# Optimization experiments

Measured on AMD Instinct MI355X. Metric: run time of the kernel, lower is better.

## Reference

```python
import jax, jax.numpy as jnp
import numpy as np

B, S, D, H, E = 4, 1024, 1024, 16, 4
HD = D // H
FF = 4 * D
EPS = 1e-5


def _ln(x):
    # normalize only; per-expert affine applied by caller
    mu = jnp.mean(x, axis=-1, keepdims=True)
    var = jnp.mean(jnp.square(x - mu), axis=-1, keepdims=True)
    return (x - mu) * jax.lax.rsqrt(var + EPS)


def setup_inputs() -> dict:
    key = jax.random.key(0)
    ks = jax.random.split(key, 12)
    s = 0.02
    inp = {
        "x": jax.random.normal(ks[0], (B, S, D), jnp.float32),
        # attention router
        "Wr_a": jax.random.normal(ks[1], (D, E), jnp.float32) * s,
        "br_a": jnp.zeros((E,), jnp.float32),
        # per-expert attention params
        "g_a": jnp.ones((E, D), jnp.float32),
        "b_a": jnp.zeros((E, D), jnp.float32),
        "Wqkv": jax.random.normal(ks[2], (E, D, 3 * D), jnp.float32) * s,
        "bqkv": jnp.zeros((E, 3 * D), jnp.float32),
        "Wpr": jax.random.normal(ks[3], (E, D, D), jnp.float32) * s,
        "bpr": jnp.zeros((E, D), jnp.float32),
        # MLP router
        "Wr_m": jax.random.normal(ks[4], (D, E), jnp.float32) * s,
        "br_m": jnp.zeros((E,), jnp.float32),
        # per-expert MLP params
        "g_m": jnp.ones((E, D), jnp.float32),
        "b_m": jnp.zeros((E, D), jnp.float32),
        "Wfc": jax.random.normal(ks[5], (E, D, FF), jnp.float32) * s,
        "bfc": jnp.zeros((E, FF), jnp.float32),
        "Wp2": jax.random.normal(ks[6], (E, FF, D), jnp.float32) * s,
        "bp2": jnp.zeros((E, D), jnp.float32),
    }
    return inp


def _block(x, Wr_a, br_a, g_a, b_a, Wqkv, bqkv, Wpr, bpr,
           Wr_m, br_m, g_m, b_m, Wfc, bfc, Wp2, bp2):
    N = B * S
    h = x.reshape(N, D)

    # ---- MoT attention (routing_all_possible_path: dense score-weighted mix) ----
    score = jax.nn.softmax(h @ Wr_a + br_a, axis=-1)          # [N,E]
    hn = _ln(h)                                                # shared normalization
    hln = hn[None, :, :] * g_a[:, None, :] + b_a[:, None, :]  # [E,N,D]
    qkv_e = jnp.einsum('end,edf->enf', hln, Wqkv) + bqkv[:, None, :]  # [E,N,3D]
    qkv = jnp.einsum('ne,enf->nf', score, qkv_e)               # [N,3D]

    q, k, v = jnp.split(qkv.reshape(B, S, 3 * D), 3, axis=-1)
    q = q.reshape(B, S, H, HD).transpose(0, 2, 1, 3)           # [B,H,S,hd]
    k = k.reshape(B, S, H, HD).transpose(0, 2, 1, 3)
    v = v.reshape(B, S, H, HD).transpose(0, 2, 1, 3)

    aw = jnp.einsum('bhqd,bhkd->bhqk', q, k) / jnp.sqrt(jnp.float32(HD))
    causal = jnp.tril(jnp.ones((S, S), bool))
    aw = jnp.where(causal, aw, jnp.finfo(aw.dtype).min)
    p = jax.nn.softmax(aw, axis=-1)
    a = jnp.einsum('bhqk,bhkd->bhqd', p, v)                    # [B,H,S,hd]
    a = a.transpose(0, 2, 1, 3).reshape(N, D)

    attn_out = jnp.einsum('ne,nd,edf->nf', score, a, Wpr) + score @ bpr
    y = x + attn_out.reshape(B, S, D)

    # ---- MoT MLP (same dense routed-expert pattern) ----
    h2 = y.reshape(N, D)
    score2 = jax.nn.softmax(h2 @ Wr_m + br_m, axis=-1)         # [N,E]
    hn2 = _ln(h2)
    hln2 = hn2[None, :, :] * g_m[:, None, :] + b_m[:, None, :]  # [E,N,D]
    inter = jax.nn.gelu(jnp.einsum('end,edf->enf', hln2, Wfc) + bfc[:, None, :])  # [E,N,FF]
    mlp_out = jnp.einsum('ne,enf,efd->nd', score2, inter, Wp2) + score2 @ bp2
    return y + mlp_out.reshape(B, S, D)


def reference(x, Wr_a, br_a, g_a, b_a, Wqkv, bqkv, Wpr, bpr,
              Wr_m, br_m, g_m, b_m, Wfc, bfc, Wp2, bp2):
    return _block(x, Wr_a, br_a, g_a, b_a, Wqkv, bqkv, Wpr, bpr,
                  Wr_m, br_m, g_m, b_m, Wfc, bfc, Wp2, bp2)
```

## Files before the change

### kernel.cpp

```cpp
#include <hip/hip_runtime.h>
#include <hip/hip_bf16.h>

typedef __bf16 bf16x8 __attribute__((ext_vector_type(8)));
typedef float f32x4 __attribute__((ext_vector_type(4)));
typedef unsigned short u16;
typedef u16 u16x8 __attribute__((ext_vector_type(8)));
typedef u16 u16x4 __attribute__((ext_vector_type(4)));

#define B_ 4
#define S_ 1024
#define D_ 1024
#define E_ 4
#define H_ 16
#define FF_ 4096
#define N_ 4096

__device__ __forceinline__ u16 f2bf(float f) {
  __hip_bfloat16 h = __float2bfloat16(f);
  return *reinterpret_cast<u16*>(&h);
}
__device__ __forceinline__ float bf2f(u16 v) {
  return __uint_as_float(((unsigned)v) << 16);
}

#define BAR()                         \
  {                                   \
    asm volatile("" ::: "memory");    \
    __builtin_amdgcn_s_barrier();     \
    asm volatile("" ::: "memory");    \
  }

__global__ __launch_bounds__(256) void tcvt(const float* __restrict__ src,
                                            u16* __restrict__ dst, int R, int C) {
  __shared__ float t[32][33];
  long base = (long)blockIdx.z * R * C;
  src += base; dst += base;
  int r0 = blockIdx.y * 32, c0 = blockIdx.x * 32;
  int tx = threadIdx.x, ty = threadIdx.y;
#pragma unroll
  for (int i = 0; i < 4; i++)
    t[ty + i * 8][tx] = src[(long)(r0 + ty + i * 8) * C + c0 + tx];
  __syncthreads();
#pragma unroll
  for (int i = 0; i < 4; i++)
    dst[(long)(c0 + ty + i * 8) * R + r0 + tx] = f2bf(t[tx][ty + i * 8]);
}

template <int YMODE, int EXPAND>
__global__ __launch_bounds__(256) void ln_router_expand(
    const float* __restrict__ X, const float* __restrict__ Wr, const float* __restrict__ br,
    const float* __restrict__ g, const float* __restrict__ bb,
    float* __restrict__ score_out, u16* __restrict__ Aout,
    long stride_e, long stride_n, int scale_flag,
    const float* __restrict__ score_a, const float* __restrict__ bpr,
    const u16* __restrict__ prt, float* __restrict__ ybuf) {
  int n = blockIdx.x, t = threadIdx.x;
  int lane = t & 63, wave = t >> 6;
  int d0 = t * 4;
  const float* xr = X + (long)n * D_;
  float4 xv = *reinterpret_cast<const float4*>(&xr[d0]);
  if (YMODE) {
    float4 sa4 = reinterpret_cast<const float4*>(score_a)[n];
    float sw[4] = {sa4.x, sa4.y, sa4.z, sa4.w};
    float4 b0 = *reinterpret_cast<const float4*>(&bpr[d0]);
    float4 b1 = *reinterpret_cast<const float4*>(&bpr[D_ + d0]);
    float4 b2 = *reinterpret_cast<const float4*>(&bpr[2 * D_ + d0]);
    float4 b3 = *reinterpret_cast<const float4*>(&bpr[3 * D_ + d0]);
    xv.x += sa4.x * b0.x + sa4.y * b1.x + sa4.z * b2.x + sa4.w * b3.x;
    xv.y += sa4.x * b0.y + sa4.y * b1.y + sa4.z * b2.y + sa4.w * b3.y;
    xv.z += sa4.x * b0.z + sa4.y * b1.z + sa4.z * b2.z + sa4.w * b3.z;
    xv.w += sa4.x * b0.w + sa4.y * b1.w + sa4.z * b2.w + sa4.w * b3.w;
    long idx = (long)n * D_ + d0;
#pragma unroll
    for (int zz = 0; zz < 4; zz++) {
      u16x4 pv = *reinterpret_cast<const u16x4*>(&prt[(long)zz * 4194304 + idx]);
      xv.x += sw[zz] * bf2f(pv[0]); xv.y += sw[zz] * bf2f(pv[1]);
      xv.z += sw[zz] * bf2f(pv[2]); xv.w += sw[zz] * bf2f(pv[3]);
    }
    *reinterpret_cast<float4*>(&ybuf[idx]) = xv;
  }
  float vals[6];
  vals[0] = xv.x + xv.y + xv.z + xv.w;
  vals[1] = xv.x * xv.x + xv.y * xv.y + xv.z * xv.z + xv.w * xv.w;
  {
    float4 w0 = reinterpret_cast<const float4*>(Wr)[d0];
    float4 w1 = reinterpret_cast<const float4*>(Wr)[d0 + 1];
    float4 w2 = reinterpret_cast<const float4*>(Wr)[d0 + 2];
    float4 w3 = reinterpret_cast<const float4*>(Wr)[d0 + 3];
    vals[2] = xv.x * w0.x + xv.y * w1.x + xv.z * w2.x + xv.w * w3.x;
    vals[3] = xv.x * w0.y + xv.y * w1.y + xv.z * w2.y + xv.w * w3.y;
    vals[4] = xv.x * w0.z + xv.y * w1.z + xv.z * w2.z + xv.w * w3.z;
    vals[5] = xv.x * w0.w + xv.y * w1.w + xv.z * w2.w + xv.w * w3.w;
  }
#pragma unroll
  for (int o = 1; o < 64; o <<= 1) {
#pragma unroll
    for (int j = 0; j < 6; j++) vals[j] += __shfl_xor(vals[j], o, 64);
  }
  __shared__ float red[4][6];
  if (lane == 0) {
#pragma unroll
    for (int j = 0; j < 6; j++) red[wave][j] = vals[j];
  }
  __syncthreads();
  float tot[6];
#pragma unroll
  for (int j = 0; j < 6; j++) tot[j] = red[0][j] + red[1][j] + red[2][j] + red[3][j];
  float mean = tot[0] * (1.0f / D_);
  float var = tot[1] * (1.0f / D_) - mean * mean;
  float rstd = rsqrtf(var + 1e-5f);
  float lg0 = tot[2] + br[0], lg1 = tot[3] + br[1], lg2 = tot[4] + br[2], lg3 = tot[5] + br[3];
  float mx = fmaxf(fmaxf(lg0, lg1), fmaxf(lg2, lg3));
  float e0 = __expf(lg0 - mx), e1 = __expf(lg1 - mx), e2 = __expf(lg2 - mx), e3 = __expf(lg3 - mx);
  float inv = 1.0f / (e0 + e1 + e2 + e3);
  float sc[4] = {e0 * inv, e1 * inv, e2 * inv, e3 * inv};
  if (t == 0) {
    float4 s4 = make_float4(sc[0], sc[1], sc[2], sc[3]);
    *reinterpret_cast<float4*>(&score_out[(long)n * 4]) = s4;
  }
  float4 hn;
  hn.x = (xv.x - mean) * rstd; hn.y = (xv.y - mean) * rstd;
  hn.z = (xv.z - mean) * rstd; hn.w = (xv.w - mean) * rstd;
  if (EXPAND) {
#pragma unroll
    for (int e = 0; e < 4; e++) {
      float4 ge = *reinterpret_cast<const float4*>(&g[e * D_ + d0]);
      float4 be = *reinterpret_cast<const float4*>(&bb[e * D_ + d0]);
      float s = scale_flag ? sc[e] : 1.0f;
      u16x4 o;
      o[0] = f2bf((hn.x * ge.x + be.x) * s);
      o[1] = f2bf((hn.y * ge.y + be.y) * s);
      o[2] = f2bf((hn.z * ge.z + be.z) * s);
      o[3] = f2bf((hn.w * ge.w + be.w) * s);
      *reinterpret_cast<u16x4*>(&Aout[(long)e * stride_e + (long)n * stride_n + d0]) = o;
    }
  } else {
    u16x4 o;
    o[0] = f2bf(hn.x); o[1] = f2bf(hn.y); o[2] = f2bf(hn.z); o[3] = f2bf(hn.w);
    *reinterpret_cast<u16x4*>(&Aout[(long)n * 1024 + d0]) = o;
  }
}

__global__ __launch_bounds__(256) void mixq(const u16* __restrict__ qp,
                                            const float* __restrict__ score_a,
                                            const float* __restrict__ bqkv,
                                            u16* __restrict__ qkvb) {
  int c = blockIdx.x * 256 + threadIdx.x;
  int n = c / 384, f0 = (c % 384) * 8;
  float4 s4 = reinterpret_cast<const float4*>(score_a)[n];
  float sw[4] = {s4.x, s4.y, s4.z, s4.w};
  float acc[8] = {};
#pragma unroll
  for (int e = 0; e < 4; e++) {
    u16x8 pv = *reinterpret_cast<const u16x8*>(&qp[(long)e * 12582912 + (long)n * 3072 + f0]);
#pragma unroll
    for (int j = 0; j < 8; j++) acc[j] += bf2f(pv[j]) + sw[e] * bqkv[e * 3072 + f0 + j];
  }
  u16x8 o;
#pragma unroll
  for (int j = 0; j < 8; j++) o[j] = f2bf(acc[j]);
  *reinterpret_cast<u16x8*>(&qkvb[(long)n * 3072 + f0]) = o;
}

template <int MODE>
__global__ __launch_bounds__(512, 2) void g8(
    const u16* __restrict__ A, const u16* __restrict__ Bt, int K, int N, int kslice,
    const float* __restrict__ score, const float* __restrict__ bias,
    u16* __restrict__ outb, int eidx, long zstride, long az, long bz) {
  __shared__ __align__(16) u16 lds0[65536];
  const int tid = threadIdx.x;
  const int w = tid >> 6, lane = tid & 63;
  const int l15 = lane & 15, l4 = lane >> 4;
  const int wr = w >> 2, wc = w & 3;

  const int gx = gridDim.x, gy = gridDim.y;
  const int total = gx * gy * gridDim.z;
  const int flat = blockIdx.x + gx * (blockIdx.y + gy * blockIdx.z);
  const int cpx = total >> 3;
  const int nf = (flat & 7) * cpx + (flat >> 3);
  const int bxi = nf % gx;
  const int tmp = nf / gx;
  const int byi = tmp % gy;
  const int z = tmp / gy;

  const long bm = (long)byi * 256, bn = (long)bxi * 256;
  const long k0 = bz ? 0L : (long)z * kslice;
  const u16* Az = bz ? (A + (long)z * az) : A;
  const u16* Btz = bz ? (Bt + (long)z * bz) : Bt;
  const int nt = kslice >> 6;

  const int cp = lane & 3;
  const int sr0 = w * 32 + (lane >> 2);
  const int sr1 = sr0 + 16;
  const int cl0 = cp ^ ((sr0 >> 1) & 3);
  const int cl1 = cp ^ ((sr1 >> 1) & 3);
  const u16* gA0 = Az + (bm + sr0) * (long)K + k0 + cl0 * 8;
  const u16* gA1 = Az + (bm + sr1) * (long)K + k0 + cl1 * 8;
  const u16* gB0 = Btz + (bn + sr0) * (long)K + k0 + cl0 * 8;
  const u16* gB1 = Btz + (bn + sr1) * (long)K + k0 + cl1 * 8;
  const int e0 = w * 1024;
  const int e1 = w * 1024 + 512;

  const int chA = l4 ^ ((l15 >> 1) & 3);
  const int rdA = (wr * 128 + l15) * 32 + chA * 8;
  const int rdB = (wc * 64 + l15) * 32 + chA * 8;

#define GLD(gsrc, ldsoff)                                                              \
  __builtin_amdgcn_global_load_lds(                                                    \
      (const __attribute__((address_space(1))) void*)(gsrc),                           \
      (__attribute__((address_space(3))) void*)(lds0 + (ldsoff)), 16, 0, 0)

  GLD(gA0, 0 + e0);
  GLD(gA1, 0 + e1);
  GLD(gB0, 16384 + e0);
  GLD(gB1, 16384 + e1);
  GLD(gA0 + 32, 8192 + e0);
  GLD(gA1 + 32, 8192 + e1);
  GLD(gB0 + 32, 24576 + e0);
  GLD(gB1 + 32, 24576 + e1);
  if (nt > 1) {
    GLD(gA0 + 64, 32768 + e0);
    GLD(gA1 + 64, 32768 + e1);
    GLD(gB0 + 64, 32768 + 16384 + e0);
    GLD(gB1 + 64, 32768 + 16384 + e1);
    GLD(gA0 + 96, 32768 + 8192 + e0);
    GLD(gA1 + 96, 32768 + 8192 + e1);
    GLD(gB0 + 96, 32768 + 24576 + e0);
    GLD(gB1 + 96, 32768 + 24576 + e1);
    asm volatile("s_waitcnt vmcnt(8)" ::: "memory");
  } else {
    asm volatile("s_waitcnt vmcnt(0)" ::: "memory");
  }
  BAR();

  f32x4 acc[8][4] = {};
  bf16x8 aC[8], bC[4], aN[8], bN[4];

#pragma unroll
  for (int i = 0; i < 8; i++) aC[i] = *(const bf16x8*)(lds0 + rdA + i * 512);
#pragma unroll
  for (int i = 0; i < 4; i++) bC[i] = *(const bf16x8*)(lds0 + 16384 + rdB + i * 512);

  for (int t = 0; t < nt; ++t) {
    const int base = (t & 1) * 32768;
    const int nb = base ^ 32768;
    const long ko2 = (long)(t + 2) * 64;
#pragma unroll
    for (int i = 0; i < 8; i++) aN[i] = *(const bf16x8*)(lds0 + base + 8192 + rdA + i * 512);
#pragma unroll
    for (int i = 0; i < 4; i++) bN[i] = *(const bf16x8*)(lds0 + base + 24576 + rdB + i * 512);
    if (t + 2 < nt) {
      GLD(gA0 + ko2, base + e0);
      GLD(gA1 + ko2, base + e1);
      GLD(gB0 + ko2, base + 16384 + e0);
      GLD(gB1 + ko2, base + 16384 + e1);
    }
    __builtin_amdgcn_s_setprio(1);
#pragma unroll
    for (int mi = 0; mi < 8; mi++)
#pragma unroll
      for (int ni = 0; ni < 4; ni++)
        acc[mi][ni] = __builtin_amdgcn_mfma_f32_16x16x32_bf16(aC[mi], bC[ni], acc[mi][ni], 0, 0, 0);
    __builtin_amdgcn_s_setprio(0);
    asm volatile("s_waitcnt lgkmcnt(0)" ::: "memory");
    if (t + 1 < nt) {
      if (t + 2 < nt) {
        asm volatile("s_waitcnt vmcnt(8)" ::: "memory");
      } else {
        asm volatile("s_waitcnt vmcnt(4)" ::: "memory");
      }
    }
    BAR();
    if (t + 1 < nt) {
#pragma unroll
      for (int i = 0; i < 8; i++) aC[i] = *(const bf16x8*)(lds0 + nb + rdA + i * 512);
#pragma unroll
      for (int i = 0; i < 4; i++) bC[i] = *(const bf16x8*)(lds0 + nb + 16384 + rdB + i * 512);
    }
    if (t + 2 < nt) {
      GLD(gA0 + ko2 + 32, base + 8192 + e0);
      GLD(gA1 + ko2 + 32, base + 8192 + e1);
      GLD(gB0 + ko2 + 32, base + 24576 + e0);
      GLD(gB1 + ko2 + 32, base + 24576 + e1);
    }
    __builtin_amdgcn_s_setprio(1);
#pragma unroll
    for (int mi = 0; mi < 8; mi++)
#pragma unroll
      for (int ni = 0; ni < 4; ni++)
        acc[mi][ni] = __builtin_amdgcn_mfma_f32_16x16x32_bf16(aN[mi], bN[ni], acc[mi][ni], 0, 0, 0);
    __builtin_amdgcn_s_setprio(0);
    asm volatile("s_waitcnt lgkmcnt(0)" ::: "memory");
    if (t + 1 < nt) {
      if (t + 2 < nt) {
        asm volatile("s_waitcnt vmcnt(8)" ::: "memory");
      } else {
        asm volatile("s_waitcnt vmcnt(0)" ::: "memory");
      }
    }
    BAR();
  }
#undef GLD

  const long zoff = (long)z * zstride;
#pragma unroll
  for (int ni = 0; ni < 4; ni++) {
    long col = bn + wc * 64 + ni * 16 + l15;
    float bcol = (MODE == 2) ? bias[col] : 0.0f;
#pragma unroll
    for (int mi = 0; mi < 8; mi++) {
#pragma unroll
      for (int r = 0; r < 4; r++) {
        long row = bm + wr * 128 + mi * 16 + l4 * 4 + r;
        float v = acc[mi][ni][r];
        if (MODE == 2) {
          float u = v + bcol;
          float zz = 0.7978845608f * (u + 0.044715f * u * u * u);
          float tt = __expf(2.0f * zz);
          float gel = u * (1.0f - 1.0f / (tt + 1.0f));
          outb[row * (long)N + col] = f2bf(gel * score[row * 4 + eidx]);
        } else {
          outb[zoff + row * (long)N + col] = f2bf(v);
        }
      }
    }
  }
}

__global__ __launch_bounds__(256) void attn_kernel(const u16* __restrict__ qkv,
                                                   u16* __restrict__ aout) {
  __shared__ __align__(16) u16 Kt[32 * 64];
  __shared__ __align__(16) u16 VT[64 * 32];
  __shared__ __align__(16) u16 Pl[4][16 * 32];
  int tid = threadIdx.x, wave = tid >> 6, lane = tid & 63;
  int l15 = lane & 15, l4 = lane >> 4;
  int qblk = blockIdx.x, bh = blockIdx.y;
  int b = bh >> 4, h = bh & 15;
  int q0 = qblk * 64 + wave * 16;
  const long LD = 3072;

  bf16x8 qf[2];
  {
    const u16* qp = qkv + (long)(b * 1024 + q0 + l15) * LD + h * 64 + l4 * 8;
    qf[0] = *(const bf16x8*)qp;
    qf[1] = *(const bf16x8*)(qp + 32);
  }
  f32x4 acc[4] = {};
  float m_run = -1e30f, l_run = 0.0f;
  int kv_end = qblk * 64 + 64;

  for (int kv0 = 0; kv0 < kv_end; kv0 += 32) {
    {
      int r = tid >> 3, c = (tid & 7) * 8;
      const u16* kp = qkv + (long)(b * 1024 + kv0 + r) * LD + 1024 + h * 64 + c;
      *(u16x8*)&Kt[r * 64 + c] = *(const u16x8*)kp;
      u16x8 vv = *(const u16x8*)(kp + 1024);
#pragma unroll
      for (int j = 0; j < 8; j++) VT[(c + j) * 32 + r] = vv[j];
    }
    __syncthreads();
    if (kv0 < q0 + 16) {
      float p[8];
      float pmax = -1e30f;
      int qg = q0 + l15;
#pragma unroll
      for (int ks = 0; ks < 2; ks++) {
        f32x4 st = {};
#pragma unroll
        for (int kc = 0; kc < 2; kc++) {
          bf16x8 kf = *(const bf16x8*)&Kt[(ks * 16 + l15) * 64 + kc * 32 + l4 * 8];
          st = __builtin_amdgcn_mfma_f32_16x16x32_bf16(kf, qf[kc], st, 0, 0, 0);
        }
#pragma unroll
        for (int r = 0; r < 4; r++) {
          int kvg = kv0 + ks * 16 + l4 * 4 + r;
          float v = st[r] * 0.125f;
          if (kvg > qg) v = -1e30f;
          p[ks * 4 + r] = v;
          pmax = fmaxf(pmax, v);
        }
      }
      pmax = fmaxf(pmax, __shfl_xor(pmax, 16, 64));
      pmax = fmaxf(pmax, __shfl_xor(pmax, 32, 64));
      float m_new = fmaxf(m_run, pmax);
      float alpha = __expf(m_run - m_new);
      float rsum = 0.f;
#pragma unroll
      for (int i = 0; i < 8; i++) {
        p[i] = __expf(p[i] - m_new);
        rsum += p[i];
      }
      rsum += __shfl_xor(rsum, 16, 64);
      rsum += __shfl_xor(rsum, 32, 64);
      l_run = l_run * alpha + rsum;
      m_run = m_new;
      float af4[4];
#pragma unroll
      for (int r = 0; r < 4; r++) af4[r] = __shfl(alpha, l4 * 4 + r, 64);
#pragma unroll
      for (int i = 0; i < 4; i++) {
#pragma unroll
        for (int r = 0; r < 4; r++) acc[i][r] *= af4[r];
      }
      u16* pw = &Pl[wave][0];
#pragma unroll
      for (int i = 0; i < 8; i++) {
        int ks = i >> 2, r = i & 3;
        pw[l15 * 32 + ks * 16 + l4 * 4 + r] = f2bf(p[i]);
      }
      bf16x8 pa = *(const bf16x8*)&pw[l15 * 32 + l4 * 8];
#pragma unroll
      for (int i = 0; i < 4; i++) {
        bf16x8 vf = *(const bf16x8*)&VT[(i * 16 + l15) * 32 + l4 * 8];
        acc[i] = __builtin_amdgcn_mfma_f32_16x16x32_bf16(pa, vf, acc[i], 0, 0, 0);
      }
    }
    __syncthreads();
  }

  float linv[4];
#pragma unroll
  for (int r = 0; r < 4; r++) {
    float lv = __shfl(l_run, l4 * 4 + r, 64);
    linv[r] = 1.0f / lv;
  }
#pragma unroll
  for (int r = 0; r < 4; r++) {
    int q = l4 * 4 + r;
    long nrow = (long)b * 1024 + q0 + q;
#pragma unroll
    for (int i = 0; i < 4; i++) {
      int d = h * 64 + i * 16 + l15;
      aout[nrow * 1024 + d] = f2bf(acc[i][r] * linv[r]);
    }
  }
}

template <int FIRST>
__global__ __launch_bounds__(256) void accum_out(const float* __restrict__ ybuf,
                                                 const float* __restrict__ score_m,
                                                 const float* __restrict__ bp2,
                                                 const u16* __restrict__ p2t,
                                                 float* __restrict__ out) {
  int n = blockIdx.x, t = threadIdx.x;
  int d0 = t * 4;
  long idx = (long)n * D_ + d0;
  float4 v;
  if (FIRST) {
    float4 s4 = reinterpret_cast<const float4*>(score_m)[n];
    float4 b0 = *reinterpret_cast<const float4*>(&bp2[d0]);
    float4 b1 = *reinterpret_cast<const float4*>(&bp2[D_ + d0]);
    float4 b2 = *reinterpret_cast<const float4*>(&bp2[2 * D_ + d0]);
    float4 b3 = *reinterpret_cast<const float4*>(&bp2[3 * D_ + d0]);
    v = *reinterpret_cast<const float4*>(&ybuf[idx]);
    v.x += s4.x * b0.x + s4.y * b1.x + s4.z * b2.x + s4.w * b3.x;
    v.y += s4.x * b0.y + s4.y * b1.y + s4.z * b2.y + s4.w * b3.y;
    v.z += s4.x * b0.z + s4.y * b1.z + s4.z * b2.z + s4.w * b3.z;
    v.w += s4.x * b0.w + s4.y * b1.w + s4.z * b2.w + s4.w * b3.w;
  } else {
    v = *reinterpret_cast<const float4*>(&out[idx]);
  }
#pragma unroll
  for (int zz = 0; zz < 4; zz++) {
    u16x4 pv = *reinterpret_cast<const u16x4*>(&p2t[(long)zz * 4194304 + idx]);
    v.x += bf2f(pv[0]); v.y += bf2f(pv[1]); v.z += bf2f(pv[2]); v.w += bf2f(pv[3]);
  }
  *reinterpret_cast<float4*>(&out[idx]) = v;
}

extern "C" void kernel_launch(void* const* d_in, const int* in_sizes, int n_in, void* d_out,
                              int out_size, void* d_ws, size_t ws_size, hipStream_t stream) {
  (void)in_sizes; (void)n_in; (void)out_size; (void)ws_size;
  const float* x    = (const float*)d_in[0];
  const float* Wr_a = (const float*)d_in[1];
  const float* br_a = (const float*)d_in[2];
  const float* g_a  = (const float*)d_in[3];
  const float* b_a  = (const float*)d_in[4];
  const float* Wqkv = (const float*)d_in[5];
  const float* bqkv = (const float*)d_in[6];
  const float* Wpr  = (const float*)d_in[7];
  const float* bpr  = (const float*)d_in[8];
  const float* Wr_m = (const float*)d_in[9];
  const float* br_m = (const float*)d_in[10];
  const float* g_m  = (const float*)d_in[11];
  const float* b_m  = (const float*)d_in[12];
  const float* Wfc  = (const float*)d_in[13];
  const float* bfc  = (const float*)d_in[14];
  const float* Wp2  = (const float*)d_in[15];
  const float* bp2  = (const float*)d_in[16];
  float* out = (float*)d_out;

  char* ws = (char*)d_ws;
  u16* wt_q   = (u16*)(ws + 0);
  u16* wt_fc  = (u16*)(ws + 0);
  u16* A_a    = (u16*)(ws + 33554432);
  u16* wt_p2  = (u16*)(ws + 33554432);
  u16* qp     = (u16*)(ws + 67108864);
  u16* A_fc   = (u16*)(ws + 67108864);
  u16* inter  = (u16*)(ws + 100663296);
  u16* p2t    = (u16*)(ws + 134217728);
  u16* qkvb   = (u16*)(ws + 167772160);
  u16* prt    = (u16*)(ws + 167772160);
  u16* abuf   = (u16*)(ws + 201326592);
  float* ybuf = (float*)(ws + 209715200);
  float* score_a = (float*)(ws + 226492416);
  float* score_m = (float*)(ws + 226492416 + 65536);

  dim3 tb(32, 8);
  tcvt<<<dim3(3072 / 32, 1024 / 32, 4), tb, 0, stream>>>(Wqkv, wt_q, 1024, 3072);
  ln_router_expand<0, 1><<<N_, 256, 0, stream>>>(x, Wr_a, br_a, g_a, b_a, score_a, A_a,
                                                 (long)4096 * 1024, (long)1024, 1,
                                                 nullptr, nullptr, nullptr, nullptr);
  g8<4><<<dim3(3072 / 256, 4096 / 256, 4), 512, 0, stream>>>(
      A_a, wt_q, 1024, 3072, 1024, nullptr, nullptr, qp, 0,
      (long)4096 * 3072, (long)4096 * 1024, (long)3072 * 1024);
  mixq<<<(4096 * 384) / 256, 256, 0, stream>>>(qp, score_a, bqkv, qkvb);
  attn_kernel<<<dim3(S_ / 64, B_ * H_), 256, 0, stream>>>(qkvb, abuf);
  u16* wt_pr = A_a;
  tcvt<<<dim3(1024 / 32, 1024 / 32, 4), tb, 0, stream>>>(Wpr, wt_pr, 1024, 1024);
  g8<4><<<dim3(1024 / 256, 4096 / 256, 4), 512, 0, stream>>>(
      abuf, wt_pr, 1024, 1024, 1024, nullptr, nullptr, prt, 0,
      (long)4096 * 1024, 0L, (long)1024 * 1024);

  tcvt<<<dim3(4096 / 32, 1024 / 32, 4), tb, 0, stream>>>(Wfc, wt_fc, 1024, 4096);
  tcvt<<<dim3(1024 / 32, 4096 / 32, 4), tb, 0, stream>>>(Wp2, wt_p2, 4096, 1024);
  ln_router_expand<1, 1><<<N_, 256, 0, stream>>>(x, Wr_m, br_m, g_m, b_m,
                                                 score_m, A_fc, (long)N_ * 1024, (long)1024,
                                                 0, score_a, bpr, prt, ybuf);
  for (int e = 0; e < 4; e++) {
    g8<2><<<dim3(4096 / 256, 4096 / 256, 1), 512, 0, stream>>>(
        A_fc + (size_t)e * N_ * 1024, wt_fc + (size_t)e * 4096 * 1024, 1024, 4096, 1024,
        score_m, bfc + e * 4096, inter, e, 0L, 0L, 0L);
    g8<4><<<dim3(1024 / 256, 4096 / 256, 4), 512, 0, stream>>>(
        inter, wt_p2 + (size_t)e * 1024 * 4096, 4096, 1024, 1024, nullptr, nullptr,
        p2t, 0, (long)4096 * 1024, 0L, 0L);
    if (e == 0) {
      accum_out<1><<<N_, 256, 0, stream>>>(ybuf, score_m, bp2, p2t, out);
    } else {
      accum_out<0><<<N_, 256, 0, stream>>>(nullptr, nullptr, nullptr, p2t, out);
    }
  }
}
```

Baseline: 783.7 us.

## Batch MLP expert GEMMs across experts with a z-dimension grid

Replaces the per-expert loop of four fc GEMMs, four projection GEMMs and four accumulate kernels with one batched launch per GEMM, using the grid z dimension over experts. The bias and score index are now selected per z, and the workspace is repacked so all expert intermediates fit at once. The aim is fewer launches and more blocks in flight per GEMM, which should improve occupancy and drop the repeated accumulation passes. The cost is a larger intermediate buffer and aliased workspace regions whose lifetimes must not overlap.

```diff
diff --git a/kernel.cpp b/kernel.cpp
--- a/kernel.cpp
+++ b/kernel.cpp
@@ -303,10 +303,12 @@
 #undef GLD
 
   const long zoff = (long)z * zstride;
+  const int ei = bz ? z : eidx;
+  const float* biasz = (MODE == 2 && bz) ? (bias + (long)z * N) : bias;
 #pragma unroll
   for (int ni = 0; ni < 4; ni++) {
     long col = bn + wc * 64 + ni * 16 + l15;
-    float bcol = (MODE == 2) ? bias[col] : 0.0f;
+    float bcol = (MODE == 2) ? biasz[col] : 0.0f;
 #pragma unroll
     for (int mi = 0; mi < 8; mi++) {
 #pragma unroll
@@ -318,7 +320,7 @@
           float zz = 0.7978845608f * (u + 0.044715f * u * u * u);
           float tt = __expf(2.0f * zz);
           float gel = u * (1.0f - 1.0f / (tt + 1.0f));
-          outb[row * (long)N + col] = f2bf(gel * score[row * 4 + eidx]);
+          outb[zoff + row * (long)N + col] = f2bf(gel * score[row * 4 + ei]);
         } else {
           outb[zoff + row * (long)N + col] = f2bf(v);
         }
@@ -491,20 +493,22 @@
   float* out = (float*)d_out;
 
   char* ws = (char*)d_ws;
+  const size_t MB = 1048576;
   u16* wt_q   = (u16*)(ws + 0);
+  u16* wt_pr  = (u16*)(ws + 0);
   u16* wt_fc  = (u16*)(ws + 0);
-  u16* A_a    = (u16*)(ws + 33554432);
-  u16* wt_p2  = (u16*)(ws + 33554432);
-  u16* qp     = (u16*)(ws + 67108864);
-  u16* A_fc   = (u16*)(ws + 67108864);
-  u16* inter  = (u16*)(ws + 100663296);
-  u16* p2t    = (u16*)(ws + 134217728);
-  u16* qkvb   = (u16*)(ws + 167772160);
-  u16* prt    = (u16*)(ws + 167772160);
-  u16* abuf   = (u16*)(ws + 201326592);
-  float* ybuf = (float*)(ws + 209715200);
-  float* score_a = (float*)(ws + 226492416);
-  float* score_m = (float*)(ws + 226492416 + 65536);
+  u16* A_a    = (u16*)(ws + 32 * MB);
+  u16* wt_p2  = (u16*)(ws + 32 * MB);
+  u16* qkvb   = (u16*)(ws + 64 * MB);
+  u16* A_fc   = (u16*)(ws + 64 * MB);
+  u16* p2t    = (u16*)(ws + 64 * MB);
+  u16* qp     = (u16*)(ws + 96 * MB);
+  u16* prt    = (u16*)(ws + 96 * MB);
+  u16* inter  = (u16*)(ws + 96 * MB);
+  u16* abuf   = (u16*)(ws + 192 * MB);
+  float* ybuf = (float*)(ws + 224 * MB);
+  float* score_a = (float*)(ws + 240 * MB);
+  float* score_m = (float*)(ws + 240 * MB + 65536);
 
   dim3 tb(32, 8);
   tcvt<<<dim3(3072 / 32, 1024 / 32, 4), tb, 0, stream>>>(Wqkv, wt_q, 1024, 3072);
@@ -516,28 +520,21 @@
       (long)4096 * 3072, (long)4096 * 1024, (long)3072 * 1024);
   mixq<<<(4096 * 384) / 256, 256, 0, stream>>>(qp, score_a, bqkv, qkvb);
   attn_kernel<<<dim3(S_ / 64, B_ * H_), 256, 0, stream>>>(qkvb, abuf);
-  u16* wt_pr = A_a;
   tcvt<<<dim3(1024 / 32, 1024 / 32, 4), tb, 0, stream>>>(Wpr, wt_pr, 1024, 1024);
   g8<4><<<dim3(1024 / 256, 4096 / 256, 4), 512, 0, stream>>>(
       abuf, wt_pr, 1024, 1024, 1024, nullptr, nullptr, prt, 0,
       (long)4096 * 1024, 0L, (long)1024 * 1024);
 
-  tcvt<<<dim3(4096 / 32, 1024 / 32, 4), tb, 0, stream>>>(Wfc, wt_fc, 1024, 4096);
-  tcvt<<<dim3(1024 / 32, 4096 / 32, 4), tb, 0, stream>>>(Wp2, wt_p2, 4096, 1024);
   ln_router_expand<1, 1><<<N_, 256, 0, stream>>>(x, Wr_m, br_m, g_m, b_m,
                                                  score_m, A_fc, (long)N_ * 1024, (long)1024,
                                                  0, score_a, bpr, prt, ybuf);
-  for (int e = 0; e < 4; e++) {
-    g8<2><<<dim3(4096 / 256, 4096 / 256, 1), 512, 0, stream>>>(
-        A_fc + (size_t)e * N_ * 1024, wt_fc + (size_t)e * 4096 * 1024, 1024, 4096, 1024,
-        score_m, bfc + e * 4096, inter, e, 0L, 0L, 0L);
-    g8<4><<<dim3(1024 / 256, 4096 / 256, 4), 512, 0, stream>>>(
-        inter, wt_p2 + (size_t)e * 1024 * 4096, 4096, 1024, 1024, nullptr, nullptr,
-        p2t, 0, (long)4096 * 1024, 0L, 0L);
-    if (e == 0) {
-      accum_out<1><<<N_, 256, 0, stream>>>(ybuf, score_m, bp2, p2t, out);
-    } else {
-      accum_out<0><<<N_, 256, 0, stream>>>(nullptr, nullptr, nullptr, p2t, out);
-    }
-  }
-}
+  tcvt<<<dim3(4096 / 32, 1024 / 32, 4), tb, 0, stream>>>(Wfc, wt_fc, 1024, 4096);
+  tcvt<<<dim3(1024 / 32, 4096 / 32, 4), tb, 0, stream>>>(Wp2, wt_p2, 4096, 1024);
+  g8<2><<<dim3(4096 / 256, 4096 / 256, 4), 512, 0, stream>>>(
+      A_fc, wt_fc, 1024, 4096, 1024, score_m, bfc, inter, 0,
+      (long)4096 * 4096, (long)N_ * 1024, (long)4096 * 1024);
+  g8<4><<<dim3(1024 / 256, 4096 / 256, 4), 512, 0, stream>>>(
+      inter, wt_p2, 4096, 1024, 4096, nullptr, nullptr, p2t, 0,
+      (long)4096 * 1024, (long)N_ * 4096, (long)1024 * 4096);
+  accum_out<1><<<N_, 256, 0, stream>>>(ybuf, score_m, bp2, p2t, out);
+}
```

Result: faster. 701.5 us (-10.5%).
